# Performance work log

Hardware: AMD Instinct MI355X
Metric: run time of the kernel (lower is better)

Reference implementation:

```python
import jax, jax.numpy as jnp
import numpy as np

EPS = 1e-5  # torch BatchNorm1d default

def setup_inputs() -> dict:
    B, I, O, F = 32, 512, 720, 321
    key = jax.random.key(0)
    k = jax.random.split(key, 7)
    x = jax.random.normal(k[0], (B, I, F), dtype=jnp.float32)
    # per-timestep Linear weights stacked: W[f] is the f-th nn.Linear (out, in)
    bound = 1.0 / np.sqrt(I)
    W = jax.random.uniform(k[1], (F, O, I), dtype=jnp.float32, minval=-bound, maxval=bound)
    b = jax.random.uniform(k[2], (F, O), dtype=jnp.float32, minval=-bound, maxval=bound)
    # BatchNorm1d(num_feats) affine params + running stats (eval-mode semantics)
    gamma = jnp.ones((F,), dtype=jnp.float32)
    beta = jnp.zeros((F,), dtype=jnp.float32)
    running_mean = jax.random.normal(k[3], (F,), dtype=jnp.float32) * 0.1
    running_var = jax.random.uniform(k[4], (F,), dtype=jnp.float32, minval=0.5, maxval=1.5)
    return {"x": x, "W": W, "b": b, "gamma": gamma, "beta": beta,
            "running_mean": running_mean, "running_var": running_var}

def reference(x, W, b, gamma, beta, running_mean, running_var):
    # x: [B, I, F]. BatchNorm1d over the feature (F) channel, applied elementwise
    # over batch and in_channels (permute/permute in torch is just a broadcast here).
    inv = gamma * jax.lax.rsqrt(running_var + EPS)          # [F]
    xn = x * inv + (beta - running_mean * inv)              # [B, I, F]
    # 321 independent Linears fused into one batched GEMM:
    # out[b, o, f] = sum_i xn[b, i, f] * W[f, o, i] + b[f, o]
    out = jnp.einsum('bif,foi->bof', xn, W) + b.T[None]     # [B, O, F]
    return out
```

## Files before the change

kernel.cpp:

```cpp
#include <hip/hip_runtime.h>
#include <stdint.h>

#define F_DIM 321
#define O_DIM 720
#define I_DIM 512
#define B_DIM 32

typedef __attribute__((ext_vector_type(8))) short short8;
typedef __attribute__((ext_vector_type(4))) float f32x4;
typedef __attribute__((ext_vector_type(4))) uint32_t u32x4;

__device__ __forceinline__ uint32_t rne_pack2(float lo, float hi) {
  uint32_t a = __builtin_bit_cast(uint32_t, lo);
  uint32_t b = __builtin_bit_cast(uint32_t, hi);
  a += 0x7FFFu + ((a >> 16) & 1u);
  b += 0x7FFFu + ((b >> 16) & 1u);
  return (a >> 16) | (b & 0xFFFF0000u);
}

__global__ void __launch_bounds__(256) xn_pack_kernel(
    const float* __restrict__ x, const float* __restrict__ gamma,
    const float* __restrict__ beta, const float* __restrict__ rmean,
    const float* __restrict__ rvar, u32x4* __restrict__ ws) {
  __shared__ float tile[8 * F_DIM];
  const int iblk = blockIdx.x;
  const int b    = blockIdx.y;
  const float* src = x + ((size_t)b * I_DIM + (size_t)iblk * 8) * F_DIM;
  for (int idx = threadIdx.x; idx < 8 * F_DIM; idx += 256)
    tile[idx] = src[idx];
  __syncthreads();
  for (int f = threadIdx.x; f < F_DIM; f += 256) {
    float inv = gamma[f] * rsqrtf(rvar[f] + 1e-5f);
    float sh  = beta[f] - rmean[f] * inv;
    float v[8];
#pragma unroll
    for (int j = 0; j < 8; ++j) v[j] = fmaf(tile[j * F_DIM + f], inv, sh);
    u32x4 pk;
    pk.x = rne_pack2(v[0], v[1]);
    pk.y = rne_pack2(v[2], v[3]);
    pk.z = rne_pack2(v[4], v[5]);
    pk.w = rne_pack2(v[6], v[7]);
    ws[(size_t)f * 2048 + iblk * 32 + b] = pk;
  }
}

__global__ void __launch_bounds__(256) linear_bn_kernel(
    const float* __restrict__ Wt, const float* __restrict__ bias,
    const u32x4* __restrict__ xn, float* __restrict__ out) {
  const int lane = threadIdx.x & 63;
  const int wv   = threadIdx.x >> 6;
  const int quad = lane >> 4;
  const int t16  = lane & 15;
  const int m0   = (wv & 1) << 4;
  const int o0   = blockIdx.x * 32 + ((wv >> 1) << 4);
  if (o0 >= O_DIM) return;
  const int fb = blockIdx.y * 4;
  const int nf = min(4, F_DIM - fb);
  const int o  = o0 + t16;

  f32x4 acc[4];
#pragma unroll
  for (int ff = 0; ff < 4; ++ff) {
    float bv = 0.0f;
    if (ff < nf) bv = bias[(size_t)(fb + ff) * O_DIM + o];
    acc[ff] = (f32x4){bv, bv, bv, bv};
  }

  for (int kk = 0; kk < 16; ++kk) {
    const int iblk = kk * 4 + quad;
#pragma unroll
    for (int ff = 0; ff < 4; ++ff) {
      if (ff < nf) {
        const int f = fb + ff;
        u32x4 av = xn[(size_t)f * 2048 + iblk * 32 + m0 + t16];
        short8 afrag = __builtin_bit_cast(short8, av);
        const float* pb =
            Wt + ((size_t)f * O_DIM + o) * I_DIM + kk * 32 + quad * 8;
        f32x4 w0 = *(const f32x4*)pb;
        f32x4 w1 = *(const f32x4*)(pb + 4);
        u32x4 bu;
        bu.x = rne_pack2(w0.x, w0.y);
        bu.y = rne_pack2(w0.z, w0.w);
        bu.z = rne_pack2(w1.x, w1.y);
        bu.w = rne_pack2(w1.z, w1.w);
        short8 bfrag = __builtin_bit_cast(short8, bu);
        acc[ff] =
            __builtin_amdgcn_mfma_f32_16x16x32_bf16(afrag, bfrag, acc[ff], 0, 0, 0);
      }
    }
  }

#pragma unroll
  for (int ff = 0; ff < 4; ++ff) {
    if (ff < nf) {
#pragma unroll
      for (int r = 0; r < 4; ++r) {
        const int brow = m0 + quad * 4 + r;
        out[((size_t)brow * O_DIM + o) * F_DIM + fb + ff] = acc[ff][r];
      }
    }
  }
}

extern "C" void kernel_launch(void* const* d_in, const int* in_sizes, int n_in,
                              void* d_out, int out_size, void* d_ws, size_t ws_size,
                              hipStream_t stream) {
  const float* x     = (const float*)d_in[0];
  const float* W     = (const float*)d_in[1];
  const float* b     = (const float*)d_in[2];
  const float* gamma = (const float*)d_in[3];
  const float* beta  = (const float*)d_in[4];
  const float* rmean = (const float*)d_in[5];
  const float* rvar  = (const float*)d_in[6];
  u32x4* ws = (u32x4*)d_ws;

  xn_pack_kernel<<<dim3(64, 32), 256, 0, stream>>>(x, gamma, beta, rmean, rvar, ws);
  linear_bn_kernel<<<dim3(23, 81), 256, 0, stream>>>(W, b, ws, (float*)d_out);
}
```

Measured before the change: 753.8 us.

## Stage W tiles through LDS with coalesced loads and register prefetch

The GEMM kernel now loads each feature's W tile (32 outputs x 512 inputs) with contiguous per-row reads, converts it to bf16, and stores it in shared memory before the MFMA loop. The next feature's tile is prefetched into registers while the current one is computed. Each block also handles 8 features instead of 4, which halves the grid. The intent is better global-load coalescing for W, the dominant byte stream, and overlap of loading with compute. The cost is two barriers per feature, 32KB of LDS per block, and more registers, which may lower occupancy.

```diff
diff --git a/kernel.cpp b/kernel.cpp
--- a/kernel.cpp
+++ b/kernel.cpp
@@ -5,6 +5,7 @@
 #define O_DIM 720
 #define I_DIM 512
 #define B_DIM 32
+#define G_F 8
 
 typedef __attribute__((ext_vector_type(8))) short short8;
 typedef __attribute__((ext_vector_type(4))) float f32x4;
@@ -47,57 +48,79 @@
 __global__ void __launch_bounds__(256) linear_bn_kernel(
     const float* __restrict__ Wt, const float* __restrict__ bias,
     const u32x4* __restrict__ xn, float* __restrict__ out) {
-  const int lane = threadIdx.x & 63;
-  const int wv   = threadIdx.x >> 6;
+  __shared__ u32x4 lds[2048];
+  const int tid  = threadIdx.x;
+  const int lane = tid & 63;
+  const int wv   = tid >> 6;
   const int quad = lane >> 4;
   const int t16  = lane & 15;
-  const int m0   = (wv & 1) << 4;
-  const int o0   = blockIdx.x * 32 + ((wv >> 1) << 4);
-  if (o0 >= O_DIM) return;
-  const int fb = blockIdx.y * 4;
-  const int nf = min(4, F_DIM - fb);
-  const int o  = o0 + t16;
+  const int mtile = wv & 1;
+  const int ntile = wv >> 1;
+  const int kkh   = wv >> 1;
+  const int ntS   = wv & 1;
+  const int o0 = blockIdx.x * 32;
+  const int fb = blockIdx.y * G_F;
+  const int nf = min(G_F, F_DIM - fb);
+  const int sRow  = ntS * 16 + (lane >> 2);
+  const int sQuad = lane & 3;
+  const int oS = min(o0 + sRow, O_DIM - 1);
+  const int oC = o0 + ntile * 16 + t16;
 
-  f32x4 acc[4];
+  f32x4 acc[G_F];
 #pragma unroll
-  for (int ff = 0; ff < 4; ++ff) {
+  for (int ff = 0; ff < G_F; ++ff) {
     float bv = 0.0f;
-    if (ff < nf) bv = bias[(size_t)(fb + ff) * O_DIM + o];
+    if (ff < nf && oC < O_DIM) bv = bias[(size_t)(fb + ff) * O_DIM + oC];
     acc[ff] = (f32x4){bv, bv, bv, bv};
   }
 
-  for (int kk = 0; kk < 16; ++kk) {
-    const int iblk = kk * 4 + quad;
+  u32x4 pk[8];
+  auto stage_load = [&](int f) {
+    const float* base =
+        Wt + ((size_t)f * O_DIM + oS) * I_DIM + kkh * 256 + sQuad * 8;
 #pragma unroll
-    for (int ff = 0; ff < 4; ++ff) {
-      if (ff < nf) {
-        const int f = fb + ff;
-        u32x4 av = xn[(size_t)f * 2048 + iblk * 32 + m0 + t16];
-        short8 afrag = __builtin_bit_cast(short8, av);
-        const float* pb =
-            Wt + ((size_t)f * O_DIM + o) * I_DIM + kk * 32 + quad * 8;
-        f32x4 w0 = *(const f32x4*)pb;
-        f32x4 w1 = *(const f32x4*)(pb + 4);
-        u32x4 bu;
-        bu.x = rne_pack2(w0.x, w0.y);
-        bu.y = rne_pack2(w0.z, w0.w);
-        bu.z = rne_pack2(w1.x, w1.y);
-        bu.w = rne_pack2(w1.z, w1.w);
-        short8 bfrag = __builtin_bit_cast(short8, bu);
-        acc[ff] =
-            __builtin_amdgcn_mfma_f32_16x16x32_bf16(afrag, bfrag, acc[ff], 0, 0, 0);
-      }
+    for (int j = 0; j < 8; ++j) {
+      f32x4 a = *(const f32x4*)(base + j * 32);
+      f32x4 b = *(const f32x4*)(base + j * 32 + 4);
+      u32x4 p;
+      p.x = rne_pack2(a.x, a.y);
+      p.y = rne_pack2(a.z, a.w);
+      p.z = rne_pack2(b.x, b.y);
+      p.w = rne_pack2(b.z, b.w);
+      pk[j] = p;
+    }
+  };
+
+  stage_load(fb);
+#pragma unroll
+  for (int ff = 0; ff < G_F; ++ff) {
+    if (ff >= nf) break;
+    __syncthreads();
+#pragma unroll
+    for (int j = 0; j < 8; ++j)
+      lds[(kkh * 8 + j) * 128 + ntS * 64 + lane] = pk[j];
+    __syncthreads();
+    if (ff + 1 < nf) stage_load(fb + ff + 1);
+    const int f = fb + ff;
+    const u32x4* xf = xn + (size_t)f * 2048 + mtile * 16 + t16;
+#pragma unroll
+    for (int kk = 0; kk < 16; ++kk) {
+      u32x4 av = xf[(kk * 4 + quad) * 32];
+      u32x4 bv = lds[kk * 128 + ntile * 64 + (t16 << 2) + quad];
+      acc[ff] = __builtin_amdgcn_mfma_f32_16x16x32_bf16(
+          __builtin_bit_cast(short8, av), __builtin_bit_cast(short8, bv),
+          acc[ff], 0, 0, 0);
     }
   }
 
+  if (oC < O_DIM) {
 #pragma unroll
-  for (int ff = 0; ff < 4; ++ff) {
-    if (ff < nf) {
+    for (int r = 0; r < 4; ++r) {
+      const int brow = mtile * 16 + quad * 4 + r;
+      float* po = out + ((size_t)brow * O_DIM + oC) * F_DIM + fb;
 #pragma unroll
-      for (int r = 0; r < 4; ++r) {
-        const int brow = m0 + quad * 4 + r;
-        out[((size_t)brow * O_DIM + o) * F_DIM + fb + ff] = acc[ff][r];
-      }
+      for (int ff = 0; ff < G_F; ++ff)
+        if (ff < nf) po[ff] = acc[ff][r];
     }
   }
 }
@@ -115,5 +138,5 @@
   u32x4* ws = (u32x4*)d_ws;
 
   xn_pack_kernel<<<dim3(64, 32), 256, 0, stream>>>(x, gamma, beta, rmean, rvar, ws);
-  linear_bn_kernel<<<dim3(23, 81), 256, 0, stream>>>(W, b, ws, (float*)d_out);
+  linear_bn_kernel<<<dim3(23, 41), 256, 0, stream>>>(W, b, ws, (float*)d_out);
 }
```

New measurement: 747.0 us. About the same (-0.9%).

## Hold activation fragments in registers and loop over output tiles per block

Applied to the files above, without the earlier changes.

The GEMM kernel now preloads each feature's full bf16 activation K-slice into registers once per block, then loops over five 16-wide output tiles, reusing those activation fragments. Blocks shrink to two waves covering two features (one wave per 16 batch rows), and the grid becomes 9x161. The goal is to cut repeated activation loads and restructure the work split so each wave streams W for many output columns. The cost is a large register footprint (32 u32x4 per thread), which may limit occupancy, and the output stores are still strided by F.

```diff
diff --git a/kernel.cpp b/kernel.cpp
--- a/kernel.cpp
+++ b/kernel.cpp
@@ -5,6 +5,7 @@
 #define O_DIM 720
 #define I_DIM 512
 #define B_DIM 32
+#define OT_PER_CHUNK 5
 
 typedef __attribute__((ext_vector_type(8))) short short8;
 typedef __attribute__((ext_vector_type(4))) float f32x4;
@@ -44,60 +45,63 @@
   }
 }
 
-__global__ void __launch_bounds__(256) linear_bn_kernel(
+__global__ void __launch_bounds__(128, 2) linear_bn_kernel(
     const float* __restrict__ Wt, const float* __restrict__ bias,
     const u32x4* __restrict__ xn, float* __restrict__ out) {
-  const int lane = threadIdx.x & 63;
-  const int wv   = threadIdx.x >> 6;
-  const int quad = lane >> 4;
-  const int t16  = lane & 15;
-  const int m0   = (wv & 1) << 4;
-  const int o0   = blockIdx.x * 32 + ((wv >> 1) << 4);
-  if (o0 >= O_DIM) return;
-  const int fb = blockIdx.y * 4;
-  const int nf = min(4, F_DIM - fb);
-  const int o  = o0 + t16;
+  const int lane  = threadIdx.x & 63;
+  const int mtile = threadIdx.x >> 6;
+  const int quad  = lane >> 4;
+  const int t16   = lane & 15;
+  const int f0 = blockIdx.y * 2;
+  const int nf = min(2, F_DIM - f0);
+  const int chunk = blockIdx.x;
 
-  f32x4 acc[4];
+  u32x4 A[2][16];
 #pragma unroll
-  for (int ff = 0; ff < 4; ++ff) {
-    float bv = 0.0f;
-    if (ff < nf) bv = bias[(size_t)(fb + ff) * O_DIM + o];
-    acc[ff] = (f32x4){bv, bv, bv, bv};
-  }
-
-  for (int kk = 0; kk < 16; ++kk) {
-    const int iblk = kk * 4 + quad;
+  for (int ff = 0; ff < 2; ++ff) {
+    if (ff < nf) {
+      const u32x4* xf = xn + (size_t)(f0 + ff) * 2048 + mtile * 16 + t16;
 #pragma unroll
-    for (int ff = 0; ff < 4; ++ff) {
-      if (ff < nf) {
-        const int f = fb + ff;
-        u32x4 av = xn[(size_t)f * 2048 + iblk * 32 + m0 + t16];
-        short8 afrag = __builtin_bit_cast(short8, av);
-        const float* pb =
-            Wt + ((size_t)f * O_DIM + o) * I_DIM + kk * 32 + quad * 8;
-        f32x4 w0 = *(const f32x4*)pb;
-        f32x4 w1 = *(const f32x4*)(pb + 4);
-        u32x4 bu;
-        bu.x = rne_pack2(w0.x, w0.y);
-        bu.y = rne_pack2(w0.z, w0.w);
-        bu.z = rne_pack2(w1.x, w1.y);
-        bu.w = rne_pack2(w1.z, w1.w);
-        short8 bfrag = __builtin_bit_cast(short8, bu);
-        acc[ff] =
-            __builtin_amdgcn_mfma_f32_16x16x32_bf16(afrag, bfrag, acc[ff], 0, 0, 0);
-      }
+      for (int kk = 0; kk < 16; ++kk)
+        A[ff][kk] = xf[(kk * 4 + quad) * 32];
     }
   }
 
+  for (int t = 0; t < OT_PER_CHUNK; ++t) {
+    const int o0 = (chunk * OT_PER_CHUNK + t) * 16;
+    const int oC = o0 + t16;
+    f32x4 acc[2];
 #pragma unroll
-  for (int ff = 0; ff < 4; ++ff) {
-    if (ff < nf) {
+    for (int ff = 0; ff < 2; ++ff) {
+      float bv = (ff < nf) ? bias[(size_t)(f0 + ff) * O_DIM + oC] : 0.0f;
+      acc[ff] = (f32x4){bv, bv, bv, bv};
+    }
 #pragma unroll
-      for (int r = 0; r < 4; ++r) {
-        const int brow = m0 + quad * 4 + r;
-        out[((size_t)brow * O_DIM + o) * F_DIM + fb + ff] = acc[ff][r];
+    for (int kk = 0; kk < 16; ++kk) {
+#pragma unroll
+      for (int ff = 0; ff < 2; ++ff) {
+        if (ff < nf) {
+          const float* pb =
+              Wt + ((size_t)(f0 + ff) * O_DIM + oC) * I_DIM + kk * 32 + quad * 8;
+          f32x4 w0 = *(const f32x4*)pb;
+          f32x4 w1 = *(const f32x4*)(pb + 4);
+          u32x4 bu;
+          bu.x = rne_pack2(w0.x, w0.y);
+          bu.y = rne_pack2(w0.z, w0.w);
+          bu.z = rne_pack2(w1.x, w1.y);
+          bu.w = rne_pack2(w1.z, w1.w);
+          acc[ff] = __builtin_amdgcn_mfma_f32_16x16x32_bf16(
+              __builtin_bit_cast(short8, A[ff][kk]),
+              __builtin_bit_cast(short8, bu), acc[ff], 0, 0, 0);
+        }
       }
+    }
+#pragma unroll
+    for (int r = 0; r < 4; ++r) {
+      const int brow = mtile * 16 + quad * 4 + r;
+      float* po = out + ((size_t)brow * O_DIM + oC) * F_DIM + f0;
+      po[0] = acc[0][r];
+      if (nf == 2) po[1] = acc[1][r];
     }
   }
 }
@@ -115,5 +119,5 @@
   u32x4* ws = (u32x4*)d_ws;
 
   xn_pack_kernel<<<dim3(64, 32), 256, 0, stream>>>(x, gamma, beta, rmean, rvar, ws);
-  linear_bn_kernel<<<dim3(23, 81), 256, 0, stream>>>(W, b, ws, (float*)d_out);
+  linear_bn_kernel<<<dim3(9, 161), 128, 0, stream>>>(W, b, ws, (float*)d_out);
 }
```

Result: slower. 814.2 us (+8.0%).
